# Kernel tuning notes

Hardware: AMD Instinct MI355X
Metric: run time of the kernel (lower is better)

## Reference

```python
import jax, jax.numpy as jnp
import numpy as np

L, B, Q, P, D, H, F = 3, 256, 128, 16, 256, 16, 512
DK = D // H
SCALE = DK ** -0.5  # lsa=False -> constant scale
EPS = 1e-5


def _ln(x, g, b):
    m = jnp.mean(x, axis=-1, keepdims=True)
    v = jnp.mean(jnp.square(x - m), axis=-1, keepdims=True)
    return (x - m) * jax.lax.rsqrt(v + EPS) * g + b


def setup_inputs() -> dict:
    key = jax.random.key(0)
    ks = jax.random.split(key, 12)
    w = lambda k, shape: 0.02 * jax.random.normal(k, shape, dtype=jnp.float32)
    return {
        "x": jax.random.normal(ks[0], (B, Q, P), dtype=jnp.float32),
        "attn_bias": 0.1 * jax.random.normal(ks[1], (1, Q, Q), dtype=jnp.float32),
        "W_P": w(ks[2], (P, D)), "b_P": jnp.zeros((D,), jnp.float32),
        "W_pos": w(ks[3], (Q, D)),
        "Wq": w(ks[4], (L, D, D)), "bq": jnp.zeros((L, D), jnp.float32),
        "Wk": w(ks[5], (L, D, D)), "bk": jnp.zeros((L, D), jnp.float32),
        "Wv": w(ks[6], (L, D, D)), "bv": jnp.zeros((L, D), jnp.float32),
        "Wo": w(ks[7], (L, D, D)), "bo": jnp.zeros((L, D), jnp.float32),
        "ln1_g": jnp.ones((L, D), jnp.float32), "ln1_b": jnp.zeros((L, D), jnp.float32),
        "W1": w(ks[8], (L, D, F)), "b1": jnp.zeros((L, F), jnp.float32),
        "W2": w(ks[9], (L, F, D)), "b2": jnp.zeros((L, D), jnp.float32),
        "ln2_g": jnp.ones((L, D), jnp.float32), "ln2_b": jnp.zeros((L, D), jnp.float32),
    }


def _encoder(x, attn_bias, W_P, b_P, W_pos,
             Wq, bq, Wk, bk, Wv, bv, Wo, bo, ln1_g, ln1_b,
             W1, b1, W2, b2, ln2_g, ln2_b):
    # patch embedding + positional encoding (dropout=0, eval mode)
    z = x @ W_P + b_P + W_pos                      # [B, Q, D]
    bias = attn_bias[:, None]                      # [1, 1, Q, Q]

    def layer(carry, p):
        z, prev = carry
        (wq, bq_, wk, bk_, wv, bv_, wo, bo_, g1, be1, w1, b1_, w2, b2_, g2, be2) = p
        q = (z @ wq + bq_).reshape(B, Q, H, DK).transpose(0, 2, 1, 3)  # [B,H,Q,dk]
        k = (z @ wk + bk_).reshape(B, Q, H, DK).transpose(0, 2, 1, 3)
        v = (z @ wv + bv_).reshape(B, Q, H, DK).transpose(0, 2, 1, 3)
        # residual-attention + bias-augmented scores
        scores = jnp.einsum('bhqd,bhkd->bhqk', q, k) * SCALE + prev + bias
        attn = jax.nn.softmax(scores, axis=-1)
        o = jnp.einsum('bhqk,bhkd->bhqd', attn, v)
        o = o.transpose(0, 2, 1, 3).reshape(B, Q, D) @ wo + bo_
        z = _ln(z + o, g1, be1)                     # post-norm
        ffo = jax.nn.gelu(z @ w1 + b1_, approximate=False) @ w2 + b2_
        z = _ln(z + ffo, g2, be2)
        return (z, scores), None

    prev0 = jnp.zeros((B, H, Q, Q), z.dtype)        # prev=None == add zero
    params = (Wq, bq, Wk, bk, Wv, bv, Wo, bo, ln1_g, ln1_b,
              W1, b1, W2, b2, ln2_g, ln2_b)
    (z, _), _ = jax.lax.scan(layer, (z, prev0), params)
    return z


def reference(x, attn_bias, W_P, b_P, W_pos, Wq, bq, Wk, bk, Wv, bv, Wo, bo,
              ln1_g, ln1_b, W1, b1, W2, b2, ln2_g, ln2_b):
    return _encoder(x, attn_bias, W_P, b_P, W_pos, Wq, bq, Wk, bk, Wv, bv,
                    Wo, bo, ln1_g, ln1_b, W1, b1, W2, b2, ln2_g, ln2_b)
```

## Files before the change

kernel.cpp:

```cpp
#include <hip/hip_runtime.h>

#define DEV __device__ __forceinline__

typedef float          f32x4  __attribute__((ext_vector_type(4)));
typedef __bf16         bf16x8 __attribute__((ext_vector_type(8)));
typedef unsigned short u16x8  __attribute__((ext_vector_type(8)));

static constexpr int  Bq   = 256;
static constexpr int  Qs   = 128;
static constexpr int  Dm   = 256;
static constexpr int  Ff   = 512;
static constexpr int  ROWS = Bq * Qs;
static constexpr long QK_LSTR = (long)ROWS * 512;

DEV float b2f(unsigned short h) {
    unsigned int u = ((unsigned int)h) << 16;
    float f; __builtin_memcpy(&f, &u, 4); return f;
}
DEV unsigned short f2b(float f) {
    unsigned int u; __builtin_memcpy(&u, &f, 4);
    u += 0x7fffu + ((u >> 16) & 1u);
    return (unsigned short)(u >> 16);
}
DEV f32x4 mfma_bf16(u16x8 a, u16x8 b, f32x4 c) {
    return __builtin_amdgcn_mfma_f32_16x16x32_bf16(
        __builtin_bit_cast(bf16x8, a), __builtin_bit_cast(bf16x8, b), c, 0, 0, 0);
}
DEV void gl_lds16(const unsigned short* g, unsigned short* l) {
    __builtin_amdgcn_global_load_lds(
        (const __attribute__((address_space(1))) unsigned int*)g,
        (__attribute__((address_space(3))) unsigned int*)l, 16, 0, 0);
}
DEV int zadr(int row, int col) {
    return row * 256 + ((((col >> 3) ^ (row & 7))) << 3) + (col & 7);
}
DEV int hadr(int row, int col) {
    return row * 512 + ((((col >> 3) ^ (row & 7))) << 3) + (col & 7);
}

__global__ void k_embed(const float* __restrict__ x,
                        const float* __restrict__ WP,
                        const float* __restrict__ bP,
                        const float* __restrict__ Wpos,
                        unsigned short* __restrict__ zb) {
    int row = blockIdx.x;
    int d   = threadIdx.x;
    int q   = row & (Qs - 1);
    const float* xr = x + row * 16;
    float acc = bP[d] + Wpos[q * Dm + d];
#pragma unroll
    for (int p = 0; p < 16; p++) acc += xr[p] * WP[p * Dm + d];
    zb[(long)row * Dm + d] = f2b(acc);
}

static constexpr int S0a = 3 * 768 * 256;
static constexpr int S0b = 3 * 768 * 256;
static constexpr int S1  = 3 * 256 * 256;
static constexpr int S2  = 3 * 512 * 256;
static constexpr int S3  = 3 * 256 * 512;
static constexpr int S4  = 3 * 768;
static constexpr int S5  = 3 * 64 * 256;
static constexpr int PREP_TOT = S0a + S0b + S1 + S2 + S3 + S4 + S5;

__global__ void k_prep(const float* __restrict__ Wq, const float* __restrict__ Wk,
                       const float* __restrict__ Wv, const float* __restrict__ Wo,
                       const float* __restrict__ W1, const float* __restrict__ W2,
                       const float* __restrict__ bq, const float* __restrict__ bk,
                       const float* __restrict__ bv, const float* __restrict__ ab,
                       unsigned short* __restrict__ wTqkv, unsigned short* __restrict__ wpQ,
                       unsigned short* __restrict__ wTo,
                       unsigned short* __restrict__ wp1, unsigned short* __restrict__ wp2,
                       float* __restrict__ bqkv, float* __restrict__ pb) {
    int idx = blockIdx.x * 256 + threadIdx.x;
    if (idx < S0a) {
        int l = idx / (768 * 256), r = idx % (768 * 256);
        int n = r / 256, k = r % 256;
        const float* W = (n < 256) ? Wq : (n < 512) ? Wk : Wv;
        float v = W[(long)l * 65536 + k * 256 + (n & 255)];
        if (n < 256) v *= 0.25f;
        wTqkv[idx] = f2b(v);
    } else if (idx < S0a + S0b) {
        int j = idx - S0a;
        int l = j / 196608, r = j % 196608;
        int tile = r >> 9, le = r & 511, lane = le >> 3, e = le & 7;
        int ntile = tile >> 3, kk = tile & 7;
        int n = ntile * 16 + (lane & 15), k = kk * 32 + (lane >> 4) * 8 + e;
        float v;
        if (n < 256)      v = Wq[(long)l * 65536 + k * 256 + n] * 0.25f;
        else if (n < 512) v = Wk[(long)l * 65536 + k * 256 + (n - 256)];
        else              v = Wv[(long)l * 65536 + k * 256 + (n - 512)];
        wpQ[j] = f2b(v);
    } else if (idx < S0a + S0b + S1) {
        int j = idx - S0a - S0b;
        int l = j / 65536, r = j % 65536, n = r / 256, k = r % 256;
        wTo[j] = f2b(Wo[(long)l * 65536 + k * 256 + n]);
    } else if (idx < S0a + S0b + S1 + S2) {
        int j = idx - S0a - S0b - S1;
        int l = j / 131072, r = j % 131072;
        int tile = r >> 9, le = r & 511, lane = le >> 3, e = le & 7;
        int ntile = tile >> 3, kk = tile & 7;
        int n = ntile * 16 + (lane & 15), k = kk * 32 + (lane >> 4) * 8 + e;
        wp1[j] = f2b(W1[(long)l * 131072 + k * 512 + n]);
    } else if (idx < S0a + S0b + S1 + S2 + S3) {
        int j = idx - S0a - S0b - S1 - S2;
        int l = j / 131072, r = j % 131072;
        int tile = r >> 9, le = r & 511, lane = le >> 3, e = le & 7;
        int ntile = tile >> 4, kk = tile & 15;
        int n = ntile * 16 + (lane & 15), k = kk * 32 + (lane >> 4) * 8 + e;
        wp2[j] = f2b(W2[(long)l * 131072 + k * 256 + n]);
    } else if (idx < S0a + S0b + S1 + S2 + S3 + S4) {
        int j = idx - S0a - S0b - S1 - S2 - S3;
        int l = j / 768, c = j % 768;
        float v = (c < 256) ? bq[l * 256 + c] * 0.25f
                : (c < 512) ? bk[l * 256 + c - 256]
                            : bv[l * 256 + c - 512];
        bqkv[j] = v;
    } else if (idx < PREP_TOT) {
        int j = idx - S0a - S0b - S1 - S2 - S3 - S4;
        int l = j / 16384, r = j % 16384;
        int u = r / 256, t = r % 256;
        int i = u >> 5, rr = (u >> 3) & 3, jj = u & 7;
        int wave = t >> 6, quad = (t >> 4) & 3, l16 = t & 15;
        int m = 32 * wave + 16 * i + 4 * quad + rr;
        int col = 16 * jj + l16;
        pb[j] = (float)(l + 1) * ab[m * 128 + col];
    }
}

template <int GELU, int MODE>
__global__ __launch_bounds__(256) void k_gemm(const unsigned short* __restrict__ A,
                                              const unsigned short* __restrict__ WT,
                                              const float* __restrict__ bias,
                                              unsigned short* __restrict__ outB,
                                              unsigned short* __restrict__ aux,
                                              int M, int N, int K) {
    __shared__ unsigned short smem[16384];
    unsigned short* As = smem;
    unsigned short* Bs = smem + 8192;
    const int tid  = threadIdx.x;
    const int wave = tid >> 6, lane = tid & 63, quad = lane >> 4, l16 = lane & 15;
    const int mq = wave >> 1, nq = wave & 1;
    const int m_blk = blockIdx.x * 128, n_blk = blockIdx.y * 128;
    const int c0 = tid, c1 = tid + 256;
    const int ra0 = c0 >> 2, ca0 = (c0 & 3) * 8;
    const int ra1 = c1 >> 2, ca1 = (c1 & 3) * 8;

    f32x4 acc[4][4] = {};

    for (int k0 = 0; k0 < K; k0 += 64) {
#pragma unroll
        for (int hh = 0; hh < 2; hh++) {
            int kk = k0 + hh * 32;
            gl_lds16(A  + (long)(m_blk + ra0) * K + kk + ca0, &As[hh * 4096 + c0 * 8]);
            gl_lds16(A  + (long)(m_blk + ra1) * K + kk + ca1, &As[hh * 4096 + c1 * 8]);
            gl_lds16(WT + (long)(n_blk + ra0) * K + kk + ca0, &Bs[hh * 4096 + c0 * 8]);
            gl_lds16(WT + (long)(n_blk + ra1) * K + kk + ca1, &Bs[hh * 4096 + c1 * 8]);
        }
        __syncthreads();
#pragma unroll
        for (int hh = 0; hh < 2; hh++) {
            u16x8 af[4], bf[4];
#pragma unroll
            for (int i = 0; i < 4; i++)
                af[i] = *(const u16x8*)&As[hh * 4096 + (64 * mq + 16 * i + l16) * 32 + quad * 8];
#pragma unroll
            for (int j = 0; j < 4; j++)
                bf[j] = *(const u16x8*)&Bs[hh * 4096 + (64 * nq + 16 * j + l16) * 32 + quad * 8];
#pragma unroll
            for (int i = 0; i < 4; i++)
#pragma unroll
                for (int j = 0; j < 4; j++)
                    acc[i][j] = mfma_bf16(af[i], bf[j], acc[i][j]);
        }
        __syncthreads();
    }

#pragma unroll
    for (int i = 0; i < 4; i++) {
        int rl = 64 * mq + 16 * i + quad * 4;
#pragma unroll
        for (int j = 0; j < 4; j++) {
            int cl = 64 * nq + 16 * j + l16;
            float bb = bias[n_blk + cl];
#pragma unroll
            for (int r = 0; r < 4; r++) {
                float v = acc[i][j][r] + bb;
                if (GELU) v = 0.5f * v * (1.0f + erff(v * 0.70710678118f));
                if (MODE == 0) smem[(rl + r) * 128 + cl] = f2b(v);
                if (MODE == 2) {
                    int g = 4 * nq + j;
                    smem[g * 2048 + (rl + r) * 16 + l16] = f2b(v);
                }
            }
        }
    }
    __syncthreads();
#pragma unroll
    for (int c = tid; c < 2048; c += 256) {
        u16x8 val = *(const u16x8*)&smem[c * 8];
        if (MODE == 0) {
            int row = c >> 4, seg = c & 15;
            *(u16x8*)&outB[(long)(m_blk + row) * N + n_blk + seg * 8] = val;
        }
        if (MODE == 2) {
            int g = c >> 8, w = c & 255;
            int n = n_blk + g * 16;
            if (n < 512) {
                int s = n >> 8, h = (n >> 4) & 15;
                *(u16x8*)&outB[((long)(((m_blk >> 7) * 16 + h) * 2 + s)) * 2048 + w * 8] = val;
            } else {
                int hh = (n - 512) >> 4;
                *(u16x8*)&aux[((long)hh * ROWS + m_blk) * 16 + w * 8] = val;
            }
        }
    }
}

template <int LAST, int AHM>
__global__ __launch_bounds__(256) void k_gemm_ln(const unsigned short* __restrict__ A,
                                                 const unsigned short* __restrict__ WT,
                                                 const float* __restrict__ bias,
                                                 const unsigned short* __restrict__ Zres,
                                                 const float* __restrict__ g,
                                                 const float* __restrict__ be,
                                                 unsigned short* __restrict__ zb,
                                                 float* __restrict__ outF,
                                                 int K) {
    __shared__ unsigned short smem[16384 + 2048 + 8192];
    unsigned short* Zs = smem;
    unsigned short* As = smem + 16384;
    unsigned short* Bs = smem + 16384 + 2048;
    float2* stats = (float2*)(smem + 16384);

    const int tid  = threadIdx.x;
    const int wave = tid >> 6, lane = tid & 63, quad = lane >> 4, l16 = lane & 15;
    const int m_blk = blockIdx.x * 64;

#pragma unroll
    for (int s = 0; s < 8; s++) {
        int c = tid + 256 * s;
        int zr = c >> 5, zc = (c & 31) * 8;
        gl_lds16(Zres + (long)(m_blk + zr) * 256 + zc, &Zs[c * 8]);
    }

    const int ca = (tid & 3) * 8, raA = tid >> 2;
    f32x4 acc[4][4] = {};

    for (int k0 = 0; k0 < K; k0 += 32) {
        if (AHM) {
            int k = k0 + ca;
            gl_lds16(A + ((long)(k >> 4) * ROWS + m_blk + raA) * 16 + (k & 15), &As[tid * 8]);
        } else {
            gl_lds16(A + (long)(m_blk + raA) * K + k0 + ca, &As[tid * 8]);
        }
#pragma unroll
        for (int s = 0; s < 4; s++) {
            int c = tid + 256 * s;
            int br = c >> 2, bc = (c & 3) * 8;
            gl_lds16(WT + (long)br * K + k0 + bc, &Bs[c * 8]);
        }
        __syncthreads();
        u16x8 af[4], bf[4];
#pragma unroll
        for (int i = 0; i < 4; i++)
            af[i] = *(const u16x8*)&As[(16 * i + l16) * 32 + quad * 8];
#pragma unroll
        for (int j = 0; j < 4; j++)
            bf[j] = *(const u16x8*)&Bs[(64 * wave + 16 * j + l16) * 32 + quad * 8];
#pragma unroll
        for (int i = 0; i < 4; i++)
#pragma unroll
            for (int j = 0; j < 4; j++)
                acc[i][j] = mfma_bf16(af[i], bf[j], acc[i][j]);
        __syncthreads();
    }

    float bb[4], gg[4], bt[4];
#pragma unroll
    for (int j = 0; j < 4; j++) {
        int col = 64 * wave + 16 * j + l16;
        bb[j] = bias[col]; gg[j] = g[col]; bt[j] = be[col];
    }
#pragma unroll
    for (int i = 0; i < 4; i++) {
#pragma unroll
        for (int r = 0; r < 4; r++) {
            int rloc = 16 * i + quad * 4 + r;
            float s1 = 0.f, s2 = 0.f;
#pragma unroll
            for (int j = 0; j < 4; j++) {
                int col = 64 * wave + 16 * j + l16;
                float v = acc[i][j][r] + bb[j] + b2f(Zs[rloc * 256 + col]);
                acc[i][j][r] = v;
                s1 += v; s2 += v * v;
            }
            for (int mk = 1; mk < 16; mk <<= 1) {
                s1 += __shfl_xor(s1, mk);
                s2 += __shfl_xor(s2, mk);
            }
            if (l16 == 0) stats[rloc * 4 + wave] = make_float2(s1, s2);
        }
    }
    __syncthreads();
#pragma unroll
    for (int i = 0; i < 4; i++) {
#pragma unroll
        for (int r = 0; r < 4; r++) {
            int rloc = 16 * i + quad * 4 + r;
            f32x4 p0 = *(const f32x4*)&stats[rloc * 4];
            f32x4 p1 = *(const f32x4*)&stats[rloc * 4 + 2];
            float S1 = p0[0] + p0[2] + p1[0] + p1[2];
            float S2 = p0[1] + p0[3] + p1[1] + p1[3];
            float mean = S1 * (1.0f / 256.0f);
            float var  = S2 * (1.0f / 256.0f) - mean * mean;
            float rstd = rsqrtf(var + 1e-5f);
            long grow = m_blk + rloc;
#pragma unroll
            for (int j = 0; j < 4; j++) {
                int col = 64 * wave + 16 * j + l16;
                float o = (acc[i][j][r] - mean) * rstd * gg[j] + bt[j];
                if (LAST) outF[grow * 256 + col] = o;
                else      zb[grow * 256 + col] = f2b(o);
            }
        }
    }
}

template <int LAST>
__global__ __launch_bounds__(256, 2) void k_ffn(
    const unsigned short* __restrict__ zin,
    const unsigned short* __restrict__ wp1, const float* __restrict__ b1,
    const unsigned short* __restrict__ wp2, const float* __restrict__ b2,
    const float* __restrict__ g2, const float* __restrict__ be2,
    unsigned short* __restrict__ zout, float* __restrict__ outF,
    const unsigned short* __restrict__ wpQ, const float* __restrict__ bqn,
    unsigned short* __restrict__ qkhn, unsigned short* __restrict__ vcurn) {
    __shared__ unsigned short Zs[32 * 256];
    __shared__ unsigned short Hs[32 * 512];
    float2* stats = (float2*)Hs;

    const int tid  = threadIdx.x;
    const int wave = tid >> 6, lane = tid & 63, quad = (lane >> 4) & 3, l16 = lane & 15;
    const int m_blk = blockIdx.x * 32;

#pragma unroll
    for (int s = 0; s < 4; s++) {
        int c = tid + 256 * s;
        int zr = c >> 5, zc = (c & 31) * 8;
        u16x8 v = *(const u16x8*)&zin[(long)(m_blk + zr) * 256 + zc];
        *(u16x8*)&Zs[zadr(zr, zc)] = v;
    }
    __syncthreads();

#pragma unroll 1
    for (int c = 0; c < 2; c++) {
        f32x4 a1[2][4] = {};
        u16x8 bf[2][4];
#pragma unroll
        for (int j = 0; j < 4; j++)
            bf[0][j] = *(const u16x8*)&wp1[((long)(16 * c + 4 * wave + j) * 8 + 0) * 512 + lane * 8];
#pragma unroll
        for (int kk = 0; kk < 8; kk++) {
            if (kk < 7)
#pragma unroll
                for (int j = 0; j < 4; j++)
                    bf[(kk + 1) & 1][j] = *(const u16x8*)&wp1[((long)(16 * c + 4 * wave + j) * 8 + kk + 1) * 512 + lane * 8];
            u16x8 af[2];
#pragma unroll
            for (int i = 0; i < 2; i++)
                af[i] = *(const u16x8*)&Zs[(16 * i + l16) * 256 + (((kk * 4 + quad) ^ (l16 & 7)) << 3)];
#pragma unroll
            for (int i = 0; i < 2; i++)
#pragma unroll
                for (int j = 0; j < 4; j++)
                    a1[i][j] = mfma_bf16(af[i], bf[kk & 1][j], a1[i][j]);
        }
        float b1v[4];
#pragma unroll
        for (int j = 0; j < 4; j++) b1v[j] = b1[256 * c + 64 * wave + 16 * j + l16];
#pragma unroll
        for (int i = 0; i < 2; i++)
#pragma unroll
            for (int j = 0; j < 4; j++)
#pragma unroll
                for (int r = 0; r < 4; r++) {
                    int row  = 16 * i + quad * 4 + r;
                    int colh = 256 * c + 64 * wave + 16 * j + l16;
                    float v = a1[i][j][r] + b1v[j];
                    float gel = 0.5f * v * (1.0f + erff(v * 0.70710678118f));
                    Hs[hadr(row, colh)] = f2b(gel);
                }
    }
    __syncthreads();

    f32x4 z2[2][4] = {};
    {
        u16x8 bg[2][4];
#pragma unroll
        for (int j = 0; j < 4; j++)
            bg[0][j] = *(const u16x8*)&wp2[((long)(4 * wave + j) * 16 + 0) * 512 + lane * 8];
#pragma unroll
        for (int kk = 0; kk < 16; kk++) {
            if (kk < 15)
#pragma unroll
                for (int j = 0; j < 4; j++)
                    bg[(kk + 1) & 1][j] = *(const u16x8*)&wp2[((long)(4 * wave + j) * 16 + kk + 1) * 512 + lane * 8];
            u16x8 af[2];
#pragma unroll
            for (int i = 0; i < 2; i++)
                af[i] = *(const u16x8*)&Hs[(16 * i + l16) * 512 + (((kk * 4 + quad) ^ (l16 & 7)) << 3)];
#pragma unroll
            for (int i = 0; i < 2; i++)
#pragma unroll
                for (int j = 0; j < 4; j++)
                    z2[i][j] = mfma_bf16(af[i], bg[kk & 1][j], z2[i][j]);
        }
    }
    __syncthreads();

    float b2v[4], gg[4], bb[4];
#pragma unroll
    for (int j = 0; j < 4; j++) {
        int col = 64 * wave + 16 * j + l16;
        b2v[j] = b2[col]; gg[j] = g2[col]; bb[j] = be2[col];
    }
#pragma unroll
    for (int i = 0; i < 2; i++)
#pragma unroll
        for (int r = 0; r < 4; r++) {
            int row = 16 * i + quad * 4 + r;
            float s1 = 0.f, s2 = 0.f;
#pragma unroll
            for (int j = 0; j < 4; j++) {
                int col = 64 * wave + 16 * j + l16;
                float v = z2[i][j][r] + b2v[j] + b2f(Zs[zadr(row, col)]);
                z2[i][j][r] = v; s1 += v; s2 += v * v;
            }
            for (int mk = 1; mk < 16; mk <<= 1) { s1 += __shfl_xor(s1, mk); s2 += __shfl_xor(s2, mk); }
            if (l16 == 0) stats[row * 4 + wave] = make_float2(s1, s2);
        }
    __syncthreads();
#pragma unroll
    for (int i = 0; i < 2; i++)
#pragma unroll
        for (int r = 0; r < 4; r++) {
            int row = 16 * i + quad * 4 + r;
            f32x4 p0 = *(const f32x4*)&stats[row * 4];
            f32x4 p1 = *(const f32x4*)&stats[row * 4 + 2];
            float S1 = p0[0] + p0[2] + p1[0] + p1[2];
            float S2 = p0[1] + p0[3] + p1[1] + p1[3];
            float mean = S1 * (1.0f / 256.0f);
            float var  = S2 * (1.0f / 256.0f) - mean * mean;
            float rstd = rsqrtf(var + 1e-5f);
            long grow = m_blk + row;
#pragma unroll
            for (int j = 0; j < 4; j++) {
                int col = 64 * wave + 16 * j + l16;
                float o = (z2[i][j][r] - mean) * rstd * gg[j] + bb[j];
                if constexpr (LAST) {
                    outF[grow * 256 + col] = o;
                } else {
                    unsigned short hv = f2b(o);
                    Zs[zadr(row, col)] = hv;
                    zout[grow * 256 + col] = hv;
                }
            }
        }

    if constexpr (!LAST) {
        __syncthreads();
        const int bb_ = m_blk >> 7;
        const int rbase = m_blk & 127;
#pragma unroll 1
        for (int p = 0; p < 3; p++) {
            f32x4 aq[2][4] = {};
            {
                u16x8 bf[2][4];
#pragma unroll
                for (int j = 0; j < 4; j++)
                    bf[0][j] = *(const u16x8*)&wpQ[((long)(16 * p + 4 * wave + j) * 8 + 0) * 512 + lane * 8];
#pragma unroll
                for (int kk = 0; kk < 8; kk++) {
                    if (kk < 7)
#pragma unroll
                        for (int j = 0; j < 4; j++)
                            bf[(kk + 1) & 1][j] = *(const u16x8*)&wpQ[((long)(16 * p + 4 * wave + j) * 8 + kk + 1) * 512 + lane * 8];
                    u16x8 af[2];
#pragma unroll
                    for (int i = 0; i < 2; i++)
                        af[i] = *(const u16x8*)&Zs[(16 * i + l16) * 256 + (((kk * 4 + quad) ^ (l16 & 7)) << 3)];
#pragma unroll
                    for (int i = 0; i < 2; i++)
#pragma unroll
                        for (int j = 0; j < 4; j++)
                            aq[i][j] = mfma_bf16(af[i], bf[kk & 1][j], aq[i][j]);
                }
            }
#pragma unroll
            for (int j = 0; j < 4; j++) {
                int col = 256 * p + 64 * wave + 16 * j + l16;
                float bqv = bqn[col];
                int h = 4 * wave + j;
                if (p < 2) {
                    unsigned short* qk = qkhn + ((long)((bb_ * 16 + h) * 2 + p)) * 2048;
#pragma unroll
                    for (int i = 0; i < 2; i++)
#pragma unroll
                        for (int r = 0; r < 4; r++) {
                            int rin = rbase + 16 * i + quad * 4 + r;
                            qk[rin * 16 + l16] = f2b(aq[i][j][r] + bqv);
                        }
                } else {
#pragma unroll
                    for (int i = 0; i < 2; i++)
#pragma unroll
                        for (int r = 0; r < 4; r++) {
                            long grow = m_blk + 16 * i + quad * 4 + r;
                            vcurn[((long)h * ROWS + grow) * 16 + l16] = f2b(aq[i][j][r] + bqv);
                        }
                }
            }
        }
    }
}

template <int L>
__global__ __launch_bounds__(256) void k_attn(const unsigned short* __restrict__ qkh,
                                              const unsigned short* __restrict__ vbuf,
                                              const float* __restrict__ pb,
                                              unsigned short* __restrict__ o_out) {
    __shared__ unsigned short vt[16 * 136];
    __shared__ unsigned short Ps[128 * 136];
    const int tid  = threadIdx.x;
    const int wave = tid >> 6, lane = tid & 63, quad = lane >> 4, l16 = lane & 15;
    const int b = blockIdx.x >> 4, h = blockIdx.x & 15;
    const int qrow = tid >> 1, half = tid & 1;

    u16x8 vv = *(const u16x8*)(vbuf + ((long)h * ROWS + b * Qs + qrow) * 16 + half * 8);
    const float* pbt = pb + (long)L * 16384 + tid;

    f32x4 accS[2][8] = {};
    u16x8 zero = {};

    constexpr int FULL = (L + 1) / 2;
    constexpr bool HALF = ((L + 1) & 1) != 0;

#pragma unroll
    for (int p = 0; p < FULL; p++) {
        const unsigned short* q0 = qkh + ((long)(((2 * p) * Bq + b) * 16 + h) * 2) * 2048;
        const unsigned short* q1 = qkh + ((long)(((2 * p + 1) * Bq + b) * 16 + h) * 2) * 2048;
        const unsigned short* qsel = (quad < 2) ? q0 : q1;
        const unsigned short* ksel = (quad < 2) ? (q0 + 2048) : (q1 + 2048);
        const int koff = (quad & 1) * 8;
        u16x8 af[2], bf8[8];
#pragma unroll
        for (int i = 0; i < 2; i++) {
            int m = 32 * wave + 16 * i + l16;
            af[i] = *(const u16x8*)(qsel + m * 16 + koff);
        }
#pragma unroll
        for (int j = 0; j < 8; j++) {
            int n = 16 * j + l16;
            bf8[j] = *(const u16x8*)(ksel + n * 16 + koff);
        }
#pragma unroll
        for (int i = 0; i < 2; i++)
#pragma unroll
            for (int j = 0; j < 8; j++)
                accS[i][j] = mfma_bf16(af[i], bf8[j], accS[i][j]);
    }
    if (HALF) {
        const unsigned short* qt = qkh + ((long)((L * Bq + b) * 16 + h) * 2) * 2048;
        const unsigned short* kt = qt + 2048;
        u16x8 af[2], bf8[8];
#pragma unroll
        for (int i = 0; i < 2; i++) {
            int m = 32 * wave + 16 * i + l16;
            af[i] = (quad < 2) ? *(const u16x8*)(qt + m * 16 + quad * 8) : zero;
        }
#pragma unroll
        for (int j = 0; j < 8; j++) {
            int n = 16 * j + l16;
            bf8[j] = (quad < 2) ? *(const u16x8*)(kt + n * 16 + quad * 8) : zero;
        }
#pragma unroll
        for (int i = 0; i < 2; i++)
#pragma unroll
            for (int j = 0; j < 8; j++)
                accS[i][j] = mfma_bf16(af[i], bf8[j], accS[i][j]);
    }

#pragma unroll
    for (int jj = 0; jj < 8; jj++) vt[(half * 8 + jj) * 136 + qrow] = vv[jj];

#pragma unroll
    for (int i = 0; i < 2; i++) {
#pragma unroll
        for (int r = 0; r < 4; r++) {
            int m = 32 * wave + 16 * i + quad * 4 + r;
#pragma unroll
            for (int j = 0; j < 8; j++) {
                int u = (i * 4 + r) * 8 + j;
                float s = accS[i][j][r] + pbt[u * 256];
                Ps[m * 136 + 16 * j + l16] = f2b(__expf(s));
            }
        }
    }
    __syncthreads();

    f32x4 accO[2] = {};
    f32x4 accR[2] = {};
    u16x8 ones;
#pragma unroll
    for (int jj = 0; jj < 8; jj++) ones[jj] = 0x3F80;
#pragma unroll
    for (int s = 0; s < 4; s++) {
        u16x8 bv = *(const u16x8*)&vt[l16 * 136 + s * 32 + quad * 8];
#pragma unroll
        for (int i = 0; i < 2; i++) {
            u16x8 ap = *(const u16x8*)&Ps[(32 * wave + 16 * i + l16) * 136 + s * 32 + quad * 8];
            accO[i] = mfma_bf16(ap, bv, accO[i]);
            accR[i] = mfma_bf16(ap, ones, accR[i]);
        }
    }
    __syncthreads();
#pragma unroll
    for (int i = 0; i < 2; i++)
#pragma unroll
        for (int r = 0; r < 4; r++) {
            int m = 32 * wave + 16 * i + quad * 4 + r;
            float inv = __builtin_amdgcn_rcpf(accR[i][r]);
            vt[m * 16 + l16] = f2b(accO[i][r] * inv);
        }
    __syncthreads();
    {
        unsigned short* obase = o_out + ((long)h * ROWS + b * Qs) * 16;
        *(u16x8*)&obase[tid * 8] = *(const u16x8*)&vt[tid * 8];
    }
}

extern "C" void kernel_launch(void* const* d_in, const int* in_sizes, int n_in,
                              void* d_out, int out_size, void* d_ws, size_t ws_size,
                              hipStream_t stream) {
    const float* x     = (const float*)d_in[0];
    const float* abias = (const float*)d_in[1];
    const float* WP    = (const float*)d_in[2];
    const float* bP    = (const float*)d_in[3];
    const float* Wpos  = (const float*)d_in[4];
    const float* Wq    = (const float*)d_in[5];
    const float* bqp   = (const float*)d_in[6];
    const float* Wk    = (const float*)d_in[7];
    const float* bkp   = (const float*)d_in[8];
    const float* Wv    = (const float*)d_in[9];
    const float* bvp   = (const float*)d_in[10];
    const float* Wo    = (const float*)d_in[11];
    const float* bo    = (const float*)d_in[12];
    const float* g1    = (const float*)d_in[13];
    const float* be1   = (const float*)d_in[14];
    const float* W1    = (const float*)d_in[15];
    const float* b1    = (const float*)d_in[16];
    const float* W2    = (const float*)d_in[17];
    const float* b2    = (const float*)d_in[18];
    const float* g2    = (const float*)d_in[19];
    const float* be2   = (const float*)d_in[20];
    (void)in_sizes; (void)n_in; (void)out_size; (void)ws_size;

    char* ws = (char*)d_ws;
    size_t off = 0;
    auto alloc = [&](size_t bytes) -> char* {
        char* p = ws + off; off += (bytes + 255) & ~(size_t)255; return p;
    };
    unsigned short* z_b   = (unsigned short*)alloc((size_t)ROWS * Dm * 2);
    unsigned short* qkh   = (unsigned short*)alloc((size_t)3 * ROWS * 512 * 2);
    unsigned short* v_cur = (unsigned short*)alloc((size_t)ROWS * Dm * 2);
    unsigned short* o_b   = (unsigned short*)alloc((size_t)ROWS * Dm * 2);
    unsigned short* wTqkv = (unsigned short*)alloc((size_t)S0a * 2);
    unsigned short* wpQ   = (unsigned short*)alloc((size_t)S0b * 2);
    unsigned short* wTo   = (unsigned short*)alloc((size_t)S1 * 2);
    unsigned short* wp1   = (unsigned short*)alloc((size_t)S2 * 2);
    unsigned short* wp2   = (unsigned short*)alloc((size_t)S3 * 2);
    float*          bqkv  = (float*)alloc((size_t)S4 * 4);
    float*          pb    = (float*)alloc((size_t)S5 * 4);

    k_prep<<<(PREP_TOT + 255) / 256, 256, 0, stream>>>(
        Wq, Wk, Wv, Wo, W1, W2, bqp, bkp, bvp, abias,
        wTqkv, wpQ, wTo, wp1, wp2, bqkv, pb);
    k_embed<<<ROWS, 256, 0, stream>>>(x, WP, bP, Wpos, z_b);

    k_gemm<0, 2><<<dim3(ROWS / 128, 6), 256, 0, stream>>>(
        z_b, wTqkv, bqkv, qkh, v_cur, ROWS, 768, 256);

    for (int l = 0; l < 3; l++) {
        if (l == 0)      k_attn<0><<<Bq * 16, 256, 0, stream>>>(qkh, v_cur, pb, o_b);
        else if (l == 1) k_attn<1><<<Bq * 16, 256, 0, stream>>>(qkh, v_cur, pb, o_b);
        else             k_attn<2><<<Bq * 16, 256, 0, stream>>>(qkh, v_cur, pb, o_b);
        k_gemm_ln<0, 1><<<ROWS / 64, 256, 0, stream>>>(
            o_b, wTo + (long)l * 256 * 256, bo + l * 256, z_b,
            g1 + l * 256, be1 + l * 256, z_b, nullptr, 256);
        if (l < 2)
            k_ffn<0><<<ROWS / 32, 256, 0, stream>>>(
                z_b, wp1 + (long)l * 131072, b1 + l * 512,
                wp2 + (long)l * 131072, b2 + l * 256,
                g2 + l * 256, be2 + l * 256, z_b, nullptr,
                wpQ + (long)(l + 1) * 196608, bqkv + (l + 1) * 768,
                qkh + (long)(l + 1) * QK_LSTR, v_cur);
        else
            k_ffn<1><<<ROWS / 32, 256, 0, stream>>>(
                z_b, wp1 + (long)l * 131072, b1 + l * 512,
                wp2 + (long)l * 131072, b2 + l * 256,
                g2 + l * 256, be2 + l * 256, nullptr, (float*)d_out,
                nullptr, nullptr, nullptr, nullptr);
    }
}
```

Before: 483.6 us.

## Fuse output projection and first LayerNorm into the FFN layer kernel

```diff
diff --git a/kernel.cpp b/kernel.cpp
--- a/kernel.cpp
+++ b/kernel.cpp
@@ -68,7 +68,7 @@
                        const float* __restrict__ bq, const float* __restrict__ bk,
                        const float* __restrict__ bv, const float* __restrict__ ab,
                        unsigned short* __restrict__ wTqkv, unsigned short* __restrict__ wpQ,
-                       unsigned short* __restrict__ wTo,
+                       unsigned short* __restrict__ wpO,
                        unsigned short* __restrict__ wp1, unsigned short* __restrict__ wp2,
                        float* __restrict__ bqkv, float* __restrict__ pb) {
     int idx = blockIdx.x * 256 + threadIdx.x;
@@ -92,8 +92,11 @@
         wpQ[j] = f2b(v);
     } else if (idx < S0a + S0b + S1) {
         int j = idx - S0a - S0b;
-        int l = j / 65536, r = j % 65536, n = r / 256, k = r % 256;
-        wTo[j] = f2b(Wo[(long)l * 65536 + k * 256 + n]);
+        int l = j / 65536, r = j % 65536;
+        int tile = r >> 9, le = r & 511, lane = le >> 3, e = le & 7;
+        int ntile = tile >> 3, kk = tile & 7;
+        int n = ntile * 16 + (lane & 15), k = kk * 32 + (lane >> 4) * 8 + e;
+        wpO[j] = f2b(Wo[(long)l * 65536 + k * 256 + n]);
     } else if (idx < S0a + S0b + S1 + S2) {
         int j = idx - S0a - S0b - S1;
         int l = j / 131072, r = j % 131072;
@@ -216,119 +219,12 @@
     }
 }
 
-template <int LAST, int AHM>
-__global__ __launch_bounds__(256) void k_gemm_ln(const unsigned short* __restrict__ A,
-                                                 const unsigned short* __restrict__ WT,
-                                                 const float* __restrict__ bias,
-                                                 const unsigned short* __restrict__ Zres,
-                                                 const float* __restrict__ g,
-                                                 const float* __restrict__ be,
-                                                 unsigned short* __restrict__ zb,
-                                                 float* __restrict__ outF,
-                                                 int K) {
-    __shared__ unsigned short smem[16384 + 2048 + 8192];
-    unsigned short* Zs = smem;
-    unsigned short* As = smem + 16384;
-    unsigned short* Bs = smem + 16384 + 2048;
-    float2* stats = (float2*)(smem + 16384);
-
-    const int tid  = threadIdx.x;
-    const int wave = tid >> 6, lane = tid & 63, quad = lane >> 4, l16 = lane & 15;
-    const int m_blk = blockIdx.x * 64;
-
-#pragma unroll
-    for (int s = 0; s < 8; s++) {
-        int c = tid + 256 * s;
-        int zr = c >> 5, zc = (c & 31) * 8;
-        gl_lds16(Zres + (long)(m_blk + zr) * 256 + zc, &Zs[c * 8]);
-    }
-
-    const int ca = (tid & 3) * 8, raA = tid >> 2;
-    f32x4 acc[4][4] = {};
-
-    for (int k0 = 0; k0 < K; k0 += 32) {
-        if (AHM) {
-            int k = k0 + ca;
-            gl_lds16(A + ((long)(k >> 4) * ROWS + m_blk + raA) * 16 + (k & 15), &As[tid * 8]);
-        } else {
-            gl_lds16(A + (long)(m_blk + raA) * K + k0 + ca, &As[tid * 8]);
-        }
-#pragma unroll
-        for (int s = 0; s < 4; s++) {
-            int c = tid + 256 * s;
-            int br = c >> 2, bc = (c & 3) * 8;
-            gl_lds16(WT + (long)br * K + k0 + bc, &Bs[c * 8]);
-        }
-        __syncthreads();
-        u16x8 af[4], bf[4];
-#pragma unroll
-        for (int i = 0; i < 4; i++)
-            af[i] = *(const u16x8*)&As[(16 * i + l16) * 32 + quad * 8];
-#pragma unroll
-        for (int j = 0; j < 4; j++)
-            bf[j] = *(const u16x8*)&Bs[(64 * wave + 16 * j + l16) * 32 + quad * 8];
-#pragma unroll
-        for (int i = 0; i < 4; i++)
-#pragma unroll
-            for (int j = 0; j < 4; j++)
-                acc[i][j] = mfma_bf16(af[i], bf[j], acc[i][j]);
-        __syncthreads();
-    }
-
-    float bb[4], gg[4], bt[4];
-#pragma unroll
-    for (int j = 0; j < 4; j++) {
-        int col = 64 * wave + 16 * j + l16;
-        bb[j] = bias[col]; gg[j] = g[col]; bt[j] = be[col];
-    }
-#pragma unroll
-    for (int i = 0; i < 4; i++) {
-#pragma unroll
-        for (int r = 0; r < 4; r++) {
-            int rloc = 16 * i + quad * 4 + r;
-            float s1 = 0.f, s2 = 0.f;
-#pragma unroll
-            for (int j = 0; j < 4; j++) {
-                int col = 64 * wave + 16 * j + l16;
-                float v = acc[i][j][r] + bb[j] + b2f(Zs[rloc * 256 + col]);
-                acc[i][j][r] = v;
-                s1 += v; s2 += v * v;
-            }
-            for (int mk = 1; mk < 16; mk <<= 1) {
-                s1 += __shfl_xor(s1, mk);
-                s2 += __shfl_xor(s2, mk);
-            }
-            if (l16 == 0) stats[rloc * 4 + wave] = make_float2(s1, s2);
-        }
-    }
-    __syncthreads();
-#pragma unroll
-    for (int i = 0; i < 4; i++) {
-#pragma unroll
-        for (int r = 0; r < 4; r++) {
-            int rloc = 16 * i + quad * 4 + r;
-            f32x4 p0 = *(const f32x4*)&stats[rloc * 4];
-            f32x4 p1 = *(const f32x4*)&stats[rloc * 4 + 2];
-            float S1 = p0[0] + p0[2] + p1[0] + p1[2];
-            float S2 = p0[1] + p0[3] + p1[1] + p1[3];
-            float mean = S1 * (1.0f / 256.0f);
-            float var  = S2 * (1.0f / 256.0f) - mean * mean;
-            float rstd = rsqrtf(var + 1e-5f);
-            long grow = m_blk + rloc;
-#pragma unroll
-            for (int j = 0; j < 4; j++) {
-                int col = 64 * wave + 16 * j + l16;
-                float o = (acc[i][j][r] - mean) * rstd * gg[j] + bt[j];
-                if (LAST) outF[grow * 256 + col] = o;
-                else      zb[grow * 256 + col] = f2b(o);
-            }
-        }
-    }
-}
-
 template <int LAST>
-__global__ __launch_bounds__(256, 2) void k_ffn(
+__global__ __launch_bounds__(256, 2) void k_layer(
     const unsigned short* __restrict__ zin,
+    const unsigned short* __restrict__ ob,
+    const unsigned short* __restrict__ wpO, const float* __restrict__ bo,
+    const float* __restrict__ g1, const float* __restrict__ be1,
     const unsigned short* __restrict__ wp1, const float* __restrict__ b1,
     const unsigned short* __restrict__ wp2, const float* __restrict__ b2,
     const float* __restrict__ g2, const float* __restrict__ be2,
@@ -347,8 +243,80 @@
     for (int s = 0; s < 4; s++) {
         int c = tid + 256 * s;
         int zr = c >> 5, zc = (c & 31) * 8;
-        u16x8 v = *(const u16x8*)&zin[(long)(m_blk + zr) * 256 + zc];
-        *(u16x8*)&Zs[zadr(zr, zc)] = v;
+        u16x8 vz = *(const u16x8*)&zin[(long)(m_blk + zr) * 256 + zc];
+        *(u16x8*)&Zs[zadr(zr, zc)] = vz;
+        int h = c >> 6, r = (c >> 1) & 31, hf = c & 1;
+        u16x8 vo = *(const u16x8*)&ob[((long)h * ROWS + m_blk + r) * 16 + hf * 8];
+        *(u16x8*)&Hs[zadr(r, h * 16 + hf * 8)] = vo;
+    }
+    __syncthreads();
+
+    f32x4 accO[2][4] = {};
+    {
+        u16x8 bf[2][4];
+#pragma unroll
+        for (int j = 0; j < 4; j++)
+            bf[0][j] = *(const u16x8*)&wpO[((long)(4 * wave + j) * 8 + 0) * 512 + lane * 8];
+#pragma unroll
+        for (int kk = 0; kk < 8; kk++) {
+            if (kk < 7)
+#pragma unroll
+                for (int j = 0; j < 4; j++)
+                    bf[(kk + 1) & 1][j] = *(const u16x8*)&wpO[((long)(4 * wave + j) * 8 + kk + 1) * 512 + lane * 8];
+            u16x8 af[2];
+#pragma unroll
+            for (int i = 0; i < 2; i++)
+                af[i] = *(const u16x8*)&Hs[(16 * i + l16) * 256 + (((kk * 4 + quad) ^ (l16 & 7)) << 3)];
+#pragma unroll
+            for (int i = 0; i < 2; i++)
+#pragma unroll
+                for (int j = 0; j < 4; j++)
+                    accO[i][j] = mfma_bf16(af[i], bf[kk & 1][j], accO[i][j]);
+        }
+    }
+    __syncthreads();
+
+    {
+        float bb[4], gg[4], bt[4];
+#pragma unroll
+        for (int j = 0; j < 4; j++) {
+            int col = 64 * wave + 16 * j + l16;
+            bb[j] = bo[col]; gg[j] = g1[col]; bt[j] = be1[col];
+        }
+#pragma unroll
+        for (int i = 0; i < 2; i++)
+#pragma unroll
+            for (int r = 0; r < 4; r++) {
+                int row = 16 * i + quad * 4 + r;
+                float s1 = 0.f, s2 = 0.f;
+#pragma unroll
+                for (int j = 0; j < 4; j++) {
+                    int col = 64 * wave + 16 * j + l16;
+                    float v = accO[i][j][r] + bb[j] + b2f(Zs[zadr(row, col)]);
+                    accO[i][j][r] = v; s1 += v; s2 += v * v;
+                }
+                for (int mk = 1; mk < 16; mk <<= 1) { s1 += __shfl_xor(s1, mk); s2 += __shfl_xor(s2, mk); }
+                if (l16 == 0) stats[row * 4 + wave] = make_float2(s1, s2);
+            }
+        __syncthreads();
+#pragma unroll
+        for (int i = 0; i < 2; i++)
+#pragma unroll
+            for (int r = 0; r < 4; r++) {
+                int row = 16 * i + quad * 4 + r;
+                f32x4 p0 = *(const f32x4*)&stats[row * 4];
+                f32x4 p1 = *(const f32x4*)&stats[row * 4 + 2];
+                float S1 = p0[0] + p0[2] + p1[0] + p1[2];
+                float S2 = p0[1] + p0[3] + p1[1] + p1[3];
+                float mean = S1 * (1.0f / 256.0f);
+                float var  = S2 * (1.0f / 256.0f) - mean * mean;
+                float rstd = rsqrtf(var + 1e-5f);
+#pragma unroll
+                for (int j = 0; j < 4; j++) {
+                    int col = 64 * wave + 16 * j + l16;
+                    Zs[zadr(row, col)] = f2b((accO[i][j][r] - mean) * rstd * gg[j] + bt[j]);
+                }
+            }
     }
     __syncthreads();
 
@@ -418,54 +386,56 @@
     }
     __syncthreads();
 
-    float b2v[4], gg[4], bb[4];
-#pragma unroll
-    for (int j = 0; j < 4; j++) {
-        int col = 64 * wave + 16 * j + l16;
-        b2v[j] = b2[col]; gg[j] = g2[col]; bb[j] = be2[col];
-    }
-#pragma unroll
-    for (int i = 0; i < 2; i++)
-#pragma unroll
-        for (int r = 0; r < 4; r++) {
-            int row = 16 * i + quad * 4 + r;
-            float s1 = 0.f, s2 = 0.f;
-#pragma unroll
-            for (int j = 0; j < 4; j++) {
-                int col = 64 * wave + 16 * j + l16;
-                float v = z2[i][j][r] + b2v[j] + b2f(Zs[zadr(row, col)]);
-                z2[i][j][r] = v; s1 += v; s2 += v * v;
-            }
-            for (int mk = 1; mk < 16; mk <<= 1) { s1 += __shfl_xor(s1, mk); s2 += __shfl_xor(s2, mk); }
-            if (l16 == 0) stats[row * 4 + wave] = make_float2(s1, s2);
-        }
-    __syncthreads();
-#pragma unroll
-    for (int i = 0; i < 2; i++)
-#pragma unroll
-        for (int r = 0; r < 4; r++) {
-            int row = 16 * i + quad * 4 + r;
-            f32x4 p0 = *(const f32x4*)&stats[row * 4];
-            f32x4 p1 = *(const f32x4*)&stats[row * 4 + 2];
-            float S1 = p0[0] + p0[2] + p1[0] + p1[2];
-            float S2 = p0[1] + p0[3] + p1[1] + p1[3];
-            float mean = S1 * (1.0f / 256.0f);
-            float var  = S2 * (1.0f / 256.0f) - mean * mean;
-            float rstd = rsqrtf(var + 1e-5f);
-            long grow = m_blk + row;
-#pragma unroll
-            for (int j = 0; j < 4; j++) {
-                int col = 64 * wave + 16 * j + l16;
-                float o = (z2[i][j][r] - mean) * rstd * gg[j] + bb[j];
-                if constexpr (LAST) {
-                    outF[grow * 256 + col] = o;
-                } else {
-                    unsigned short hv = f2b(o);
-                    Zs[zadr(row, col)] = hv;
-                    zout[grow * 256 + col] = hv;
-                }
-            }
-        }
+    {
+        float b2v[4], gg[4], bb[4];
+#pragma unroll
+        for (int j = 0; j < 4; j++) {
+            int col = 64 * wave + 16 * j + l16;
+            b2v[j] = b2[col]; gg[j] = g2[col]; bb[j] = be2[col];
+        }
+#pragma unroll
+        for (int i = 0; i < 2; i++)
+#pragma unroll
+            for (int r = 0; r < 4; r++) {
+                int row = 16 * i + quad * 4 + r;
+                float s1 = 0.f, s2 = 0.f;
+#pragma unroll
+                for (int j = 0; j < 4; j++) {
+                    int col = 64 * wave + 16 * j + l16;
+                    float v = z2[i][j][r] + b2v[j] + b2f(Zs[zadr(row, col)]);
+                    z2[i][j][r] = v; s1 += v; s2 += v * v;
+                }
+                for (int mk = 1; mk < 16; mk <<= 1) { s1 += __shfl_xor(s1, mk); s2 += __shfl_xor(s2, mk); }
+                if (l16 == 0) stats[row * 4 + wave] = make_float2(s1, s2);
+            }
+        __syncthreads();
+#pragma unroll
+        for (int i = 0; i < 2; i++)
+#pragma unroll
+            for (int r = 0; r < 4; r++) {
+                int row = 16 * i + quad * 4 + r;
+                f32x4 p0 = *(const f32x4*)&stats[row * 4];
+                f32x4 p1 = *(const f32x4*)&stats[row * 4 + 2];
+                float S1 = p0[0] + p0[2] + p1[0] + p1[2];
+                float S2 = p0[1] + p0[3] + p1[1] + p1[3];
+                float mean = S1 * (1.0f / 256.0f);
+                float var  = S2 * (1.0f / 256.0f) - mean * mean;
+                float rstd = rsqrtf(var + 1e-5f);
+                long grow = m_blk + row;
+#pragma unroll
+                for (int j = 0; j < 4; j++) {
+                    int col = 64 * wave + 16 * j + l16;
+                    float o = (z2[i][j][r] - mean) * rstd * gg[j] + bb[j];
+                    if constexpr (LAST) {
+                        outF[grow * 256 + col] = o;
+                    } else {
+                        unsigned short hv = f2b(o);
+                        Zs[zadr(row, col)] = hv;
+                        zout[grow * 256 + col] = hv;
+                    }
+                }
+            }
+    }
 
     if constexpr (!LAST) {
         __syncthreads();
@@ -676,7 +646,7 @@
     unsigned short* o_b   = (unsigned short*)alloc((size_t)ROWS * Dm * 2);
     unsigned short* wTqkv = (unsigned short*)alloc((size_t)S0a * 2);
     unsigned short* wpQ   = (unsigned short*)alloc((size_t)S0b * 2);
-    unsigned short* wTo   = (unsigned short*)alloc((size_t)S1 * 2);
+    unsigned short* wpO   = (unsigned short*)alloc((size_t)S1 * 2);
     unsigned short* wp1   = (unsigned short*)alloc((size_t)S2 * 2);
     unsigned short* wp2   = (unsigned short*)alloc((size_t)S3 * 2);
     float*          bqkv  = (float*)alloc((size_t)S4 * 4);
@@ -684,7 +654,7 @@
 
     k_prep<<<(PREP_TOT + 255) / 256, 256, 0, stream>>>(
         Wq, Wk, Wv, Wo, W1, W2, bqp, bkp, bvp, abias,
-        wTqkv, wpQ, wTo, wp1, wp2, bqkv, pb);
+        wTqkv, wpQ, wpO, wp1, wp2, bqkv, pb);
     k_embed<<<ROWS, 256, 0, stream>>>(x, WP, bP, Wpos, z_b);
 
     k_gemm<0, 2><<<dim3(ROWS / 128, 6), 256, 0, stream>>>(
@@ -694,19 +664,20 @@
         if (l == 0)      k_attn<0><<<Bq * 16, 256, 0, stream>>>(qkh, v_cur, pb, o_b);
         else if (l == 1) k_attn<1><<<Bq * 16, 256, 0, stream>>>(qkh, v_cur, pb, o_b);
         else             k_attn<2><<<Bq * 16, 256, 0, stream>>>(qkh, v_cur, pb, o_b);
-        k_gemm_ln<0, 1><<<ROWS / 64, 256, 0, stream>>>(
-            o_b, wTo + (long)l * 256 * 256, bo + l * 256, z_b,
-            g1 + l * 256, be1 + l * 256, z_b, nullptr, 256);
         if (l < 2)
-            k_ffn<0><<<ROWS / 32, 256, 0, stream>>>(
-                z_b, wp1 + (long)l * 131072, b1 + l * 512,
+            k_layer<0><<<ROWS / 32, 256, 0, stream>>>(
+                z_b, o_b, wpO + (long)l * 65536, bo + l * 256,
+                g1 + l * 256, be1 + l * 256,
+                wp1 + (long)l * 131072, b1 + l * 512,
                 wp2 + (long)l * 131072, b2 + l * 256,
                 g2 + l * 256, be2 + l * 256, z_b, nullptr,
                 wpQ + (long)(l + 1) * 196608, bqkv + (l + 1) * 768,
                 qkh + (long)(l + 1) * QK_LSTR, v_cur);
         else
-            k_ffn<1><<<ROWS / 32, 256, 0, stream>>>(
-                z_b, wp1 + (long)l * 131072, b1 + l * 512,
+            k_layer<1><<<ROWS / 32, 256, 0, stream>>>(
+                z_b, o_b, wpO + (long)l * 65536, bo + l * 256,
+                g1 + l * 256, be1 + l * 256,
+                wp1 + (long)l * 131072, b1 + l * 512,
                 wp2 + (long)l * 131072, b2 + l * 256,
                 g2 + l * 256, be2 + l * 256, nullptr, (float*)d_out,
                 nullptr, nullptr, nullptr, nullptr);
```

Result: slower. 585.1 us (+21.0%).
